# Performance work log

Measured on AMD Instinct MI355X. Metric: run time of the kernel, lower is better.

The kernel has to match this reference:

```python
import jax, jax.numpy as jnp
import numpy as np

LN_EPS = 1e-5
B, N, D, V = 2048, 8, 1024, 4096


def setup_inputs() -> dict:
    key = jax.random.key(0)
    k1, k2, k3, k4 = jax.random.split(key, 4)
    return {
        "input_embedding": jax.random.normal(k1, (B, D), dtype=jnp.float32),
        "features": jax.random.randint(k2, (B, N), 0, V, dtype=jnp.int64),
        "embed_tables": jax.random.normal(k3, (N, V, D), dtype=jnp.float32) * 0.02,
        "W_pred": jax.random.normal(k4, (N, D, V), dtype=jnp.float32) * 0.02,
        "b_pred": jnp.zeros((N, V), dtype=jnp.float32),
        "ln_gamma": jnp.ones((D,), dtype=jnp.float32),
        "ln_beta": jnp.zeros((D,), dtype=jnp.float32),
    }


def reference(input_embedding, features, embed_tables, W_pred, b_pred, ln_gamma, ln_beta):
    # Per-feature embedding lookup: embed_tables[n, features[b,n]] -> [B, N, D]
    feat_emb = embed_tables[jnp.arange(N)[None, :], features]
    # Stack input embedding in front: [B, N+1, D]
    embeddings = jnp.concatenate([input_embedding[:, None, :], feat_emb], axis=1)
    # Original: triu(diag=1) mask-multiply-sum then [:, 1:, :].
    # masked_sums[:, t] = sum_{s < t} emb[:, s]; slicing t=1..N == inclusive cumsum
    # over the first N positions.
    masked_sums = jnp.cumsum(embeddings, axis=1)[:, :-1, :]  # [B, N, D]
    # LayerNorm over last dim
    mu = jnp.mean(masked_sums, axis=-1, keepdims=True)
    var = jnp.var(masked_sums, axis=-1, keepdims=True)
    h = (masked_sums - mu) / jnp.sqrt(var + LN_EPS) * ln_gamma + ln_beta
    # Exact (erf) GELU, matching nn.GELU default
    h = jax.nn.gelu(h, approximate=False)
    # Per-feature predictor heads as one batched GEMM: [B, N, V]
    logits = jnp.einsum("bnd,ndv->bnv", h, W_pred) + b_pred
    return logits
```

## Files before the change

### kernel.cpp

```cpp
#include <hip/hip_runtime.h>
#include <hip/hip_bf16.h>

#define B_ 2048
#define N_ 8
#define D_ 1024
#define V_ 4096
#define LN_EPS_ 1e-5f

#define BM 128
#define BN 128
#define BK 32

typedef __bf16 bf16x8 __attribute__((ext_vector_type(8)));
typedef float f32x4 __attribute__((ext_vector_type(4)));

#define GLB(p) ((const __attribute__((address_space(1))) void*)(p))
#define LDSP(p) ((__attribute__((address_space(3))) void*)(p))

static __device__ __forceinline__ unsigned short f2bf(float x) {
    union { float f; unsigned int u; } v;
    v.f = x;
    unsigned int r = v.u + 0x7fffu + ((v.u >> 16) & 1u);
    return (unsigned short)(r >> 16);
}

__global__ __launch_bounds__(256) void wconv(const float* __restrict__ W,
                                             unsigned short* __restrict__ Wt) {
    __shared__ unsigned short tile[64][65];
    const int n  = blockIdx.z;
    const int v0 = blockIdx.x * 64;
    const int d0 = blockIdx.y * 64;
    const int tx = threadIdx.x;
    const int ty = threadIdx.y;
#pragma unroll
    for (int i = 0; i < 4; ++i) {
        const int d = ty + i * 16;
        const float4 w4 = *(const float4*)&W[((size_t)n * D_ + d0 + d) * V_ + v0 + tx * 4];
        tile[d][tx * 4 + 0] = f2bf(w4.x);
        tile[d][tx * 4 + 1] = f2bf(w4.y);
        tile[d][tx * 4 + 2] = f2bf(w4.z);
        tile[d][tx * 4 + 3] = f2bf(w4.w);
    }
    __syncthreads();
#pragma unroll
    for (int i = 0; i < 4; ++i) {
        const int v = ty + i * 16;
        ushort4 pk;
        pk.x = tile[tx * 4 + 0][v];
        pk.y = tile[tx * 4 + 1][v];
        pk.z = tile[tx * 4 + 2][v];
        pk.w = tile[tx * 4 + 3][v];
        *reinterpret_cast<ushort4*>(&Wt[((size_t)n * V_ + v0 + v) * D_ + d0 + tx * 4]) = pk;
    }
}

__global__ __launch_bounds__(256) void stage1(const float* __restrict__ ie,
                                              const int* __restrict__ feats,
                                              const float* __restrict__ emb,
                                              const float* __restrict__ gamma,
                                              const float* __restrict__ beta,
                                              unsigned short* __restrict__ H) {
    const int b = blockIdx.x;
    const int t = threadIdx.x;
    const int d0 = t * 4;
    const int lane = t & 63, wid = t >> 6;

    float4 s  = *(const float4*)&ie[(size_t)b * D_ + d0];
    const float4 g4 = *(const float4*)&gamma[d0];
    const float4 be4 = *(const float4*)&beta[d0];

    int fc[N_];
#pragma unroll
    for (int n = 0; n < N_; ++n) fc[n] = feats[b * N_ + n];

    __shared__ float redS[4], redQ[4];

#pragma unroll
    for (int n = 0; n < N_; ++n) {
        float ls = s.x + s.y + s.z + s.w;
        float lq = s.x * s.x + s.y * s.y + s.z * s.z + s.w * s.w;
#pragma unroll
        for (int off = 32; off > 0; off >>= 1) {
            ls += __shfl_down(ls, off, 64);
            lq += __shfl_down(lq, off, 64);
        }
        if (lane == 0) { redS[wid] = ls; redQ[wid] = lq; }
        __syncthreads();
        const float tot  = redS[0] + redS[1] + redS[2] + redS[3];
        const float totq = redQ[0] + redQ[1] + redQ[2] + redQ[3];
        __syncthreads();

        const float mu   = tot * (1.0f / D_);
        const float var  = totq * (1.0f / D_) - mu * mu;
        const float rstd = rsqrtf(var + LN_EPS_);

        float h0 = (s.x - mu) * rstd * g4.x + be4.x;
        float h1 = (s.y - mu) * rstd * g4.y + be4.y;
        float h2 = (s.z - mu) * rstd * g4.z + be4.z;
        float h3 = (s.w - mu) * rstd * g4.w + be4.w;
        h0 = 0.5f * h0 * (1.0f + erff(h0 * 0.70710678f));
        h1 = 0.5f * h1 * (1.0f + erff(h1 * 0.70710678f));
        h2 = 0.5f * h2 * (1.0f + erff(h2 * 0.70710678f));
        h3 = 0.5f * h3 * (1.0f + erff(h3 * 0.70710678f));

        ushort4 pk;
        pk.x = f2bf(h0); pk.y = f2bf(h1); pk.z = f2bf(h2); pk.w = f2bf(h3);
        *reinterpret_cast<ushort4*>(&H[((size_t)n * B_ + b) * D_ + d0]) = pk;

        const float4 e = *(const float4*)&emb[((size_t)n * V_ + fc[n]) * (size_t)D_ + d0];
        s.x += e.x; s.y += e.y; s.z += e.z; s.w += e.w;
    }
}

__global__ __launch_bounds__(256) void gemm(const unsigned short* __restrict__ H,
                                            const unsigned short* __restrict__ Wt,
                                            const float* __restrict__ bp,
                                            float* __restrict__ out) {
    const int vt = blockIdx.x;
    const int mt = blockIdx.y;
    const int n  = blockIdx.z;
    const int t = threadIdx.x;
    const int wid = t >> 6, lane = t & 63;
    const int wr = wid >> 1, wc = wid & 1;

    __shared__ unsigned short shA[BM * BK];
    __shared__ unsigned short shB[BN * BK];
    char* ldsA = (char*)shA;
    char* ldsB = (char*)shB;

    const unsigned short* Abase = H  + ((size_t)n * B_ + (size_t)mt * BM) * D_;
    const unsigned short* Bbase = Wt + ((size_t)n * V_ + (size_t)vt * BN) * D_;

    const int row0 = t >> 2;
    const int ks   = t & 3;

    f32x4 acc[4][4] = {};

    for (int kt = 0; kt < D_; kt += BK) {
        __builtin_amdgcn_global_load_lds(GLB(Abase + (size_t)row0 * D_ + kt + ks * 8),
                                         LDSP(ldsA + t * 16), 16, 0, 0);
        __builtin_amdgcn_global_load_lds(GLB(Abase + (size_t)(row0 + 64) * D_ + kt + ks * 8),
                                         LDSP(ldsA + 4096 + t * 16), 16, 0, 0);
        __builtin_amdgcn_global_load_lds(GLB(Bbase + (size_t)row0 * D_ + kt + ks * 8),
                                         LDSP(ldsB + t * 16), 16, 0, 0);
        __builtin_amdgcn_global_load_lds(GLB(Bbase + (size_t)(row0 + 64) * D_ + kt + ks * 8),
                                         LDSP(ldsB + 4096 + t * 16), 16, 0, 0);
        __syncthreads();

        const int lrow = lane & 15;
        const int lk   = (lane >> 4) * 16;
        bf16x8 af[4], bf[4];
#pragma unroll
        for (int i = 0; i < 4; ++i)
            af[i] = *reinterpret_cast<const bf16x8*>(ldsA + (wr * 64 + i * 16 + lrow) * 64 + lk);
#pragma unroll
        for (int i = 0; i < 4; ++i)
            bf[i] = *reinterpret_cast<const bf16x8*>(ldsB + (wc * 64 + i * 16 + lrow) * 64 + lk);
#pragma unroll
        for (int i = 0; i < 4; ++i)
#pragma unroll
            for (int j = 0; j < 4; ++j)
                acc[i][j] = __builtin_amdgcn_mfma_f32_16x16x32_bf16(af[i], bf[j], acc[i][j], 0, 0, 0);
        __syncthreads();
    }

    const int col  = lane & 15;
    const int rgrp = (lane >> 4) * 4;
    float bias[4];
#pragma unroll
    for (int j = 0; j < 4; ++j)
        bias[j] = bp[(size_t)n * V_ + vt * BN + wc * 64 + j * 16 + col];
#pragma unroll
    for (int i = 0; i < 4; ++i) {
        const int grow = mt * BM + wr * 64 + i * 16 + rgrp;
#pragma unroll
        for (int j = 0; j < 4; ++j) {
            const int gcol = vt * BN + wc * 64 + j * 16 + col;
#pragma unroll
            for (int r = 0; r < 4; ++r) {
                out[((size_t)(grow + r) * N_ + n) * V_ + gcol] = acc[i][j][r] + bias[j];
            }
        }
    }
}

extern "C" void kernel_launch(void* const* d_in, const int* in_sizes, int n_in,
                              void* d_out, int out_size, void* d_ws, size_t ws_size,
                              hipStream_t stream) {
    const float* ie  = (const float*)d_in[0];
    const int*   fts = (const int*)d_in[1];
    const float* emb = (const float*)d_in[2];
    const float* W   = (const float*)d_in[3];
    const float* bp  = (const float*)d_in[4];
    const float* gam = (const float*)d_in[5];
    const float* bet = (const float*)d_in[6];
    float* out = (float*)d_out;

    unsigned short* Wt = (unsigned short*)d_ws;
    unsigned short* H  = (unsigned short*)((char*)d_ws + (size_t)N_ * V_ * D_ * 2);

    wconv<<<dim3(V_ / 64, D_ / 64, N_), dim3(16, 16), 0, stream>>>(W, Wt);
    stage1<<<dim3(B_), dim3(256), 0, stream>>>(ie, fts, emb, gam, bet, H);
    gemm<<<dim3(V_ / BN, B_ / BM, N_), dim3(256), 0, stream>>>(H, Wt, bp, out);
}
```

Measured before the change: 284.5 us.

## Replace GEMM with 256x256 double-buffered, swizzled, 8-wave pipelined MFMA kernel

Swaps the simple 128x128x32 single-buffered GEMM for a 256x256x64 tile kernel with 512 threads. The kernel double-buffers through 128KB of dynamic LDS, issues the next tile's global-to-LDS loads interleaved with MFMA phases using explicit vmcnt waits and barriers, and XOR-swizzles the LDS layout to avoid bank conflicts. It also raises wave priority around MFMA blocks. The aim is to hide memory latency and raise arithmetic intensity, at the cost of more LDS, register pressure and fragile hand-placed wait counts.

```diff
diff --git a/kernel.cpp b/kernel.cpp
--- a/kernel.cpp
+++ b/kernel.cpp
@@ -6,10 +6,6 @@
 #define D_ 1024
 #define V_ 4096
 #define LN_EPS_ 1e-5f
-
-#define BM 128
-#define BN 128
-#define BK 32
 
 typedef __bf16 bf16x8 __attribute__((ext_vector_type(8)));
 typedef float f32x4 __attribute__((ext_vector_type(4)));
@@ -112,73 +108,123 @@
     }
 }
 
-__global__ __launch_bounds__(256) void gemm(const unsigned short* __restrict__ H,
-                                            const unsigned short* __restrict__ Wt,
-                                            const float* __restrict__ bp,
-                                            float* __restrict__ out) {
-    const int vt = blockIdx.x;
-    const int mt = blockIdx.y;
-    const int n  = blockIdx.z;
+#define MF(a, b, c) __builtin_amdgcn_mfma_f32_16x16x32_bf16((a), (b), (c), 0, 0, 0)
+
+#define STG_A(u, kt, bb) __builtin_amdgcn_global_load_lds( \
+    GLB(Ab + (size_t)((u) * 64 + srow) * D_ + (kt) + gsl), \
+    LDSP(lds + (bb) + (u) * 8192 + t * 16), 16, 0, 0)
+#define STG_B(u, kt, bb) __builtin_amdgcn_global_load_lds( \
+    GLB(Bb + (size_t)((u) * 64 + srow) * D_ + (kt) + gsl), \
+    LDSP(lds + (bb) + 32768 + (u) * 8192 + t * 16), 16, 0, 0)
+
+#define RD_A(i, ks, bb) (*(const bf16x8*)(lds + (bb) + ((i) >> 1) * 8192 + \
+    (((i) & 1) * 32 + wr * 16 + lrow) * 128 + ((((ks) * 4 + lkq) ^ sw) * 16)))
+#define RD_B(j, ks, bb) (*(const bf16x8*)(lds + (bb) + 32768 + wc * 8192 + \
+    ((j) * 16 + lrow) * 128 + ((((ks) * 4 + lkq) ^ sw) * 16)))
+
+#define QUADP(i0, i1) \
+    _Pragma("unroll") for (int j = 0; j < 4; ++j) { \
+        acc[i0][j] = MF(A00, Bf[j][0], acc[i0][j]); \
+        acc[i0][j] = MF(A01, Bf[j][1], acc[i0][j]); \
+        acc[i1][j] = MF(A10, Bf[j][0], acc[i1][j]); \
+        acc[i1][j] = MF(A11, Bf[j][1], acc[i1][j]); \
+    }
+
+#define TILE(KT, bc, bn) { \
+    bf16x8 Bf[4][2]; \
+    asm volatile("s_waitcnt vmcnt(3)" ::: "memory"); \
+    __builtin_amdgcn_s_barrier(); \
+    _Pragma("unroll") for (int j = 0; j < 4; ++j) { Bf[j][0] = RD_B(j, 0, bc); Bf[j][1] = RD_B(j, 1, bc); } \
+    { bf16x8 A00 = RD_A(0, 0, bc), A01 = RD_A(0, 1, bc), A10 = RD_A(1, 0, bc), A11 = RD_A(1, 1, bc); \
+      STG_B(0, (KT) + 64, bn); STG_B(1, (KT) + 64, bn); \
+      __builtin_amdgcn_s_setprio(1); QUADP(0, 1); __builtin_amdgcn_s_setprio(0); } \
+    asm volatile("s_waitcnt vmcnt(4)" ::: "memory"); \
+    __builtin_amdgcn_s_barrier(); \
+    { bf16x8 A00 = RD_A(2, 0, bc), A01 = RD_A(2, 1, bc), A10 = RD_A(3, 0, bc), A11 = RD_A(3, 1, bc); \
+      STG_B(2, (KT) + 64, bn); STG_B(3, (KT) + 64, bn); \
+      __builtin_amdgcn_s_setprio(1); QUADP(2, 3); __builtin_amdgcn_s_setprio(0); } \
+    asm volatile("s_waitcnt vmcnt(4)" ::: "memory"); \
+    __builtin_amdgcn_s_barrier(); \
+    { bf16x8 A00 = RD_A(4, 0, bc), A01 = RD_A(4, 1, bc), A10 = RD_A(5, 0, bc), A11 = RD_A(5, 1, bc); \
+      STG_A(0, (KT) + 64, bn); STG_A(1, (KT) + 64, bn); \
+      __builtin_amdgcn_s_setprio(1); QUADP(4, 5); __builtin_amdgcn_s_setprio(0); } \
+    asm volatile("s_waitcnt vmcnt(6)" ::: "memory"); \
+    __builtin_amdgcn_s_barrier(); \
+    { bf16x8 A00 = RD_A(6, 0, bc), A01 = RD_A(6, 1, bc), A10 = RD_A(7, 0, bc), A11 = RD_A(7, 1, bc); \
+      STG_A(2, (KT) + 64, bn); STG_A(3, (KT) + 64, bn); \
+      __builtin_amdgcn_s_setprio(1); QUADP(6, 7); __builtin_amdgcn_s_setprio(0); } \
+}
+
+#define TILE_LAST(bc) { \
+    bf16x8 Bf[4][2]; \
+    asm volatile("s_waitcnt vmcnt(3)" ::: "memory"); \
+    __builtin_amdgcn_s_barrier(); \
+    _Pragma("unroll") for (int j = 0; j < 4; ++j) { Bf[j][0] = RD_B(j, 0, bc); Bf[j][1] = RD_B(j, 1, bc); } \
+    { bf16x8 A00 = RD_A(0, 0, bc), A01 = RD_A(0, 1, bc), A10 = RD_A(1, 0, bc), A11 = RD_A(1, 1, bc); \
+      __builtin_amdgcn_s_setprio(1); QUADP(0, 1); __builtin_amdgcn_s_setprio(0); } \
+    asm volatile("s_waitcnt vmcnt(2)" ::: "memory"); \
+    __builtin_amdgcn_s_barrier(); \
+    { bf16x8 A00 = RD_A(2, 0, bc), A01 = RD_A(2, 1, bc), A10 = RD_A(3, 0, bc), A11 = RD_A(3, 1, bc); \
+      __builtin_amdgcn_s_setprio(1); QUADP(2, 3); __builtin_amdgcn_s_setprio(0); } \
+    asm volatile("s_waitcnt vmcnt(1)" ::: "memory"); \
+    __builtin_amdgcn_s_barrier(); \
+    { bf16x8 A00 = RD_A(4, 0, bc), A01 = RD_A(4, 1, bc), A10 = RD_A(5, 0, bc), A11 = RD_A(5, 1, bc); \
+      __builtin_amdgcn_s_setprio(1); QUADP(4, 5); __builtin_amdgcn_s_setprio(0); } \
+    asm volatile("s_waitcnt vmcnt(0)" ::: "memory"); \
+    __builtin_amdgcn_s_barrier(); \
+    { bf16x8 A00 = RD_A(6, 0, bc), A01 = RD_A(6, 1, bc), A10 = RD_A(7, 0, bc), A11 = RD_A(7, 1, bc); \
+      __builtin_amdgcn_s_setprio(1); QUADP(6, 7); __builtin_amdgcn_s_setprio(0); } \
+}
+
+__global__ __launch_bounds__(512, 2) void gemm8(const unsigned short* __restrict__ H,
+                                                const unsigned short* __restrict__ Wt,
+                                                const float* __restrict__ bp,
+                                                float* __restrict__ out) {
+    extern __shared__ char lds[];
+    const int vt = blockIdx.x, mt = blockIdx.y, n = blockIdx.z;
     const int t = threadIdx.x;
     const int wid = t >> 6, lane = t & 63;
-    const int wr = wid >> 1, wc = wid & 1;
-
-    __shared__ unsigned short shA[BM * BK];
-    __shared__ unsigned short shB[BN * BK];
-    char* ldsA = (char*)shA;
-    char* ldsB = (char*)shB;
-
-    const unsigned short* Abase = H  + ((size_t)n * B_ + (size_t)mt * BM) * D_;
-    const unsigned short* Bbase = Wt + ((size_t)n * V_ + (size_t)vt * BN) * D_;
-
-    const int row0 = t >> 2;
-    const int ks   = t & 3;
-
-    f32x4 acc[4][4] = {};
-
-    for (int kt = 0; kt < D_; kt += BK) {
-        __builtin_amdgcn_global_load_lds(GLB(Abase + (size_t)row0 * D_ + kt + ks * 8),
-                                         LDSP(ldsA + t * 16), 16, 0, 0);
-        __builtin_amdgcn_global_load_lds(GLB(Abase + (size_t)(row0 + 64) * D_ + kt + ks * 8),
-                                         LDSP(ldsA + 4096 + t * 16), 16, 0, 0);
-        __builtin_amdgcn_global_load_lds(GLB(Bbase + (size_t)row0 * D_ + kt + ks * 8),
-                                         LDSP(ldsB + t * 16), 16, 0, 0);
-        __builtin_amdgcn_global_load_lds(GLB(Bbase + (size_t)(row0 + 64) * D_ + kt + ks * 8),
-                                         LDSP(ldsB + 4096 + t * 16), 16, 0, 0);
-        __syncthreads();
-
-        const int lrow = lane & 15;
-        const int lk   = (lane >> 4) * 16;
-        bf16x8 af[4], bf[4];
-#pragma unroll
-        for (int i = 0; i < 4; ++i)
-            af[i] = *reinterpret_cast<const bf16x8*>(ldsA + (wr * 64 + i * 16 + lrow) * 64 + lk);
-#pragma unroll
-        for (int i = 0; i < 4; ++i)
-            bf[i] = *reinterpret_cast<const bf16x8*>(ldsB + (wc * 64 + i * 16 + lrow) * 64 + lk);
-#pragma unroll
-        for (int i = 0; i < 4; ++i)
-#pragma unroll
-            for (int j = 0; j < 4; ++j)
-                acc[i][j] = __builtin_amdgcn_mfma_f32_16x16x32_bf16(af[i], bf[j], acc[i][j], 0, 0, 0);
-        __syncthreads();
-    }
-
-    const int col  = lane & 15;
-    const int rgrp = (lane >> 4) * 4;
+    const int wr = wid >> 2, wc = wid & 3;
+
+    const unsigned short* Ab = H  + ((size_t)n * B_ + (size_t)mt * 256) * D_;
+    const unsigned short* Bb = Wt + ((size_t)n * V_ + (size_t)vt * 256) * D_;
+
+    const int srow = t >> 3;
+    const int gsl  = ((t & 7) ^ (srow & 7)) * 8;
+
+    const int lrow = lane & 15;
+    const int lkq  = lane >> 4;
+    const int sw   = lane & 7;
+
+    f32x4 acc[8][4] = {};
+
+    STG_B(0, 0, 0); STG_B(1, 0, 0); STG_B(2, 0, 0); STG_B(3, 0, 0);
+    STG_A(0, 0, 0); STG_A(1, 0, 0); STG_A(2, 0, 0); STG_A(3, 0, 0);
+
+    int kt = 0;
+#pragma unroll 1
+    for (int it = 0; it < 7; ++it) {
+        TILE(kt, 0, 65536); kt += 64;
+        TILE(kt, 65536, 0); kt += 64;
+    }
+    TILE(kt, 0, 65536);
+    TILE_LAST(65536);
+
+    const int col = lane & 15;
+    const int rg  = (lane >> 4) * 4;
+    const int gc0 = vt * 256 + wc * 64 + col;
     float bias[4];
 #pragma unroll
-    for (int j = 0; j < 4; ++j)
-        bias[j] = bp[(size_t)n * V_ + vt * BN + wc * 64 + j * 16 + col];
-#pragma unroll
-    for (int i = 0; i < 4; ++i) {
-        const int grow = mt * BM + wr * 64 + i * 16 + rgrp;
+    for (int j = 0; j < 4; ++j) bias[j] = bp[(size_t)n * V_ + gc0 + j * 16];
+#pragma unroll
+    for (int i = 0; i < 8; ++i) {
+        const int row = mt * 256 + i * 32 + wr * 16 + rg;
 #pragma unroll
         for (int j = 0; j < 4; ++j) {
-            const int gcol = vt * BN + wc * 64 + j * 16 + col;
+            const int gcol = gc0 + j * 16;
 #pragma unroll
             for (int r = 0; r < 4; ++r) {
-                out[((size_t)(grow + r) * N_ + n) * V_ + gcol] = acc[i][j][r] + bias[j];
+                out[((size_t)(row + r) * N_ + n) * V_ + gcol] = acc[i][j][r] + bias[j];
             }
         }
     }
@@ -199,7 +245,10 @@
     unsigned short* Wt = (unsigned short*)d_ws;
     unsigned short* H  = (unsigned short*)((char*)d_ws + (size_t)N_ * V_ * D_ * 2);
 
+    (void)hipFuncSetAttribute(reinterpret_cast<const void*>(gemm8),
+                              hipFuncAttributeMaxDynamicSharedMemorySize, 131072);
+
     wconv<<<dim3(V_ / 64, D_ / 64, N_), dim3(16, 16), 0, stream>>>(W, Wt);
     stage1<<<dim3(B_), dim3(256), 0, stream>>>(ie, fts, emb, gam, bet, H);
-    gemm<<<dim3(V_ / BN, B_ / BM, N_), dim3(256), 0, stream>>>(H, Wt, bp, out);
-}
+    gemm8<<<dim3(V_ / 256, B_ / 256, N_), 512, 131072, stream>>>(H, Wt, bp, out);
+}
```

New measurement: 254.0 us. -10.7%, faster.

## Fuse prep kernels and rewrite GEMM with 256x256 tiles and 4-stage LDS pipeline

Applied to the files above, without the earlier changes.

Merges the weight-conversion and LayerNorm/GELU kernels into one launch, using block-index ranges to pick the role. Replaces the 128x128 single-buffered GEMM with a 512-thread 256x256 tile kernel. The new GEMM keeps a 4-deep ring of direct-to-LDS loads with partial vmcnt waits, XOR-swizzles the LDS layout to avoid bank conflicts, raises MFMA issue priority, and remaps block IDs for better L2 locality. The aim is to hide global-memory latency and raise operand reuse, at the cost of 128KB of dynamic LDS per block and heavy register pressure.

```diff
diff --git a/kernel.cpp b/kernel.cpp
--- a/kernel.cpp
+++ b/kernel.cpp
@@ -7,10 +7,6 @@
 #define V_ 4096
 #define LN_EPS_ 1e-5f
 
-#define BM 128
-#define BN 128
-#define BK 32
-
 typedef __bf16 bf16x8 __attribute__((ext_vector_type(8)));
 typedef float f32x4 __attribute__((ext_vector_type(4)));
 
@@ -24,162 +20,189 @@
     return (unsigned short)(r >> 16);
 }
 
-__global__ __launch_bounds__(256) void wconv(const float* __restrict__ W,
-                                             unsigned short* __restrict__ Wt) {
-    __shared__ unsigned short tile[64][65];
-    const int n  = blockIdx.z;
-    const int v0 = blockIdx.x * 64;
-    const int d0 = blockIdx.y * 64;
-    const int tx = threadIdx.x;
-    const int ty = threadIdx.y;
-#pragma unroll
-    for (int i = 0; i < 4; ++i) {
-        const int d = ty + i * 16;
-        const float4 w4 = *(const float4*)&W[((size_t)n * D_ + d0 + d) * V_ + v0 + tx * 4];
-        tile[d][tx * 4 + 0] = f2bf(w4.x);
-        tile[d][tx * 4 + 1] = f2bf(w4.y);
-        tile[d][tx * 4 + 2] = f2bf(w4.z);
-        tile[d][tx * 4 + 3] = f2bf(w4.w);
+__global__ __launch_bounds__(256) void prep(const float* __restrict__ ie,
+                                            const int* __restrict__ feats,
+                                            const float* __restrict__ emb,
+                                            const float* __restrict__ gamma,
+                                            const float* __restrict__ beta,
+                                            const float* __restrict__ W,
+                                            unsigned short* __restrict__ H,
+                                            unsigned short* __restrict__ Wt) {
+    const int bid = blockIdx.x;
+    const int t = threadIdx.x;
+
+    if (bid >= 2048) {
+        __shared__ unsigned short tile[64][65];
+        const int w  = bid - 2048;
+        const int v0 = (w & 63) * 64;
+        const int d0 = ((w >> 6) & 15) * 64;
+        const int n  = w >> 10;
+        const int tx = t & 15, ty = t >> 4;
+#pragma unroll
+        for (int i = 0; i < 4; ++i) {
+            const int d = ty + i * 16;
+            const float4 w4 = *(const float4*)&W[((size_t)n * D_ + d0 + d) * V_ + v0 + tx * 4];
+            tile[d][tx * 4 + 0] = f2bf(w4.x);
+            tile[d][tx * 4 + 1] = f2bf(w4.y);
+            tile[d][tx * 4 + 2] = f2bf(w4.z);
+            tile[d][tx * 4 + 3] = f2bf(w4.w);
+        }
+        __syncthreads();
+#pragma unroll
+        for (int i = 0; i < 4; ++i) {
+            const int v = ty + i * 16;
+            ushort4 pk;
+            pk.x = tile[tx * 4 + 0][v];
+            pk.y = tile[tx * 4 + 1][v];
+            pk.z = tile[tx * 4 + 2][v];
+            pk.w = tile[tx * 4 + 3][v];
+            *reinterpret_cast<ushort4*>(&Wt[((size_t)n * V_ + v0 + v) * D_ + d0 + tx * 4]) = pk;
+        }
+    } else {
+        __shared__ float redS[4], redQ[4];
+        const int b = bid;
+        const int d0 = t * 4;
+        const int lane = t & 63, wid = t >> 6;
+
+        float4 s  = *(const float4*)&ie[(size_t)b * D_ + d0];
+        const float4 g4 = *(const float4*)&gamma[d0];
+        const float4 be4 = *(const float4*)&beta[d0];
+
+        int fc[N_];
+#pragma unroll
+        for (int n = 0; n < N_; ++n) fc[n] = feats[b * N_ + n];
+
+#pragma unroll
+        for (int n = 0; n < N_; ++n) {
+            float ls = s.x + s.y + s.z + s.w;
+            float lq = s.x * s.x + s.y * s.y + s.z * s.z + s.w * s.w;
+#pragma unroll
+            for (int off = 32; off > 0; off >>= 1) {
+                ls += __shfl_down(ls, off, 64);
+                lq += __shfl_down(lq, off, 64);
+            }
+            if (lane == 0) { redS[wid] = ls; redQ[wid] = lq; }
+            __syncthreads();
+            const float tot  = redS[0] + redS[1] + redS[2] + redS[3];
+            const float totq = redQ[0] + redQ[1] + redQ[2] + redQ[3];
+            __syncthreads();
+
+            const float mu   = tot * (1.0f / D_);
+            const float var  = totq * (1.0f / D_) - mu * mu;
+            const float rstd = rsqrtf(var + LN_EPS_);
+
+            float h0 = (s.x - mu) * rstd * g4.x + be4.x;
+            float h1 = (s.y - mu) * rstd * g4.y + be4.y;
+            float h2 = (s.z - mu) * rstd * g4.z + be4.z;
+            float h3 = (s.w - mu) * rstd * g4.w + be4.w;
+            h0 = 0.5f * h0 * (1.0f + erff(h0 * 0.70710678f));
+            h1 = 0.5f * h1 * (1.0f + erff(h1 * 0.70710678f));
+            h2 = 0.5f * h2 * (1.0f + erff(h2 * 0.70710678f));
+            h3 = 0.5f * h3 * (1.0f + erff(h3 * 0.70710678f));
+
+            ushort4 pk;
+            pk.x = f2bf(h0); pk.y = f2bf(h1); pk.z = f2bf(h2); pk.w = f2bf(h3);
+            *reinterpret_cast<ushort4*>(&H[((size_t)n * B_ + b) * D_ + d0]) = pk;
+
+            const float4 e = *(const float4*)&emb[((size_t)n * V_ + fc[n]) * (size_t)D_ + d0];
+            s.x += e.x; s.y += e.y; s.z += e.z; s.w += e.w;
+        }
     }
-    __syncthreads();
-#pragma unroll
-    for (int i = 0; i < 4; ++i) {
-        const int v = ty + i * 16;
-        ushort4 pk;
-        pk.x = tile[tx * 4 + 0][v];
-        pk.y = tile[tx * 4 + 1][v];
-        pk.z = tile[tx * 4 + 2][v];
-        pk.w = tile[tx * 4 + 3][v];
-        *reinterpret_cast<ushort4*>(&Wt[((size_t)n * V_ + v0 + v) * D_ + d0 + tx * 4]) = pk;
-    }
-}
-
-__global__ __launch_bounds__(256) void stage1(const float* __restrict__ ie,
-                                              const int* __restrict__ feats,
-                                              const float* __restrict__ emb,
-                                              const float* __restrict__ gamma,
-                                              const float* __restrict__ beta,
-                                              unsigned short* __restrict__ H) {
-    const int b = blockIdx.x;
-    const int t = threadIdx.x;
-    const int d0 = t * 4;
-    const int lane = t & 63, wid = t >> 6;
-
-    float4 s  = *(const float4*)&ie[(size_t)b * D_ + d0];
-    const float4 g4 = *(const float4*)&gamma[d0];
-    const float4 be4 = *(const float4*)&beta[d0];
-
-    int fc[N_];
-#pragma unroll
-    for (int n = 0; n < N_; ++n) fc[n] = feats[b * N_ + n];
-
-    __shared__ float redS[4], redQ[4];
-
-#pragma unroll
-    for (int n = 0; n < N_; ++n) {
-        float ls = s.x + s.y + s.z + s.w;
-        float lq = s.x * s.x + s.y * s.y + s.z * s.z + s.w * s.w;
-#pragma unroll
-        for (int off = 32; off > 0; off >>= 1) {
-            ls += __shfl_down(ls, off, 64);
-            lq += __shfl_down(lq, off, 64);
-        }
-        if (lane == 0) { redS[wid] = ls; redQ[wid] = lq; }
-        __syncthreads();
-        const float tot  = redS[0] + redS[1] + redS[2] + redS[3];
-        const float totq = redQ[0] + redQ[1] + redQ[2] + redQ[3];
-        __syncthreads();
-
-        const float mu   = tot * (1.0f / D_);
-        const float var  = totq * (1.0f / D_) - mu * mu;
-        const float rstd = rsqrtf(var + LN_EPS_);
-
-        float h0 = (s.x - mu) * rstd * g4.x + be4.x;
-        float h1 = (s.y - mu) * rstd * g4.y + be4.y;
-        float h2 = (s.z - mu) * rstd * g4.z + be4.z;
-        float h3 = (s.w - mu) * rstd * g4.w + be4.w;
-        h0 = 0.5f * h0 * (1.0f + erff(h0 * 0.70710678f));
-        h1 = 0.5f * h1 * (1.0f + erff(h1 * 0.70710678f));
-        h2 = 0.5f * h2 * (1.0f + erff(h2 * 0.70710678f));
-        h3 = 0.5f * h3 * (1.0f + erff(h3 * 0.70710678f));
-
-        ushort4 pk;
-        pk.x = f2bf(h0); pk.y = f2bf(h1); pk.z = f2bf(h2); pk.w = f2bf(h3);
-        *reinterpret_cast<ushort4*>(&H[((size_t)n * B_ + b) * D_ + d0]) = pk;
-
-        const float4 e = *(const float4*)&emb[((size_t)n * V_ + fc[n]) * (size_t)D_ + d0];
-        s.x += e.x; s.y += e.y; s.z += e.z; s.w += e.w;
-    }
-}
-
-__global__ __launch_bounds__(256) void gemm(const unsigned short* __restrict__ H,
-                                            const unsigned short* __restrict__ Wt,
-                                            const float* __restrict__ bp,
-                                            float* __restrict__ out) {
-    const int vt = blockIdx.x;
-    const int mt = blockIdx.y;
-    const int n  = blockIdx.z;
+}
+
+#define MF(a, b, c) __builtin_amdgcn_mfma_f32_16x16x32_bf16((a), (b), (c), 0, 0, 0)
+
+#define STAGE(As, Bs, bb) { \
+    __builtin_amdgcn_global_load_lds(GLB((As) + (size_t)srow * D_ + gsl),         LDSP(lds + (bb) + t * 16), 16, 0, 0); \
+    __builtin_amdgcn_global_load_lds(GLB((As) + (size_t)(srow + 128) * D_ + gsl), LDSP(lds + (bb) + 8192 + t * 16), 16, 0, 0); \
+    __builtin_amdgcn_global_load_lds(GLB((Bs) + (size_t)srow * D_ + gsl),         LDSP(lds + (bb) + 16384 + t * 16), 16, 0, 0); \
+    __builtin_amdgcn_global_load_lds(GLB((Bs) + (size_t)(srow + 128) * D_ + gsl), LDSP(lds + (bb) + 24576 + t * 16), 16, 0, 0); \
+}
+
+#define RD_A(i, bb) (*(const bf16x8*)(lds + (bb) + ((i) * 32 + wr * 16 + lrow) * 64 + swk))
+#define RD_B(j, bb) (*(const bf16x8*)(lds + (bb) + 16384 + (wc * 64 + (j) * 16 + lrow) * 64 + swk))
+
+#define TILE1(bc, bn, As, Bs) { \
+    asm volatile("s_waitcnt vmcnt(8)" ::: "memory"); \
+    __builtin_amdgcn_s_barrier(); \
+    STAGE(As, Bs, bn); \
+    bf16x8 Bf[4], Af[4]; \
+    _Pragma("unroll") for (int j = 0; j < 4; ++j) Bf[j] = RD_B(j, bc); \
+    _Pragma("unroll") for (int i = 0; i < 4; ++i) Af[i] = RD_A(i, bc); \
+    __builtin_amdgcn_s_setprio(1); \
+    _Pragma("unroll") for (int i = 0; i < 4; ++i) \
+        _Pragma("unroll") for (int j = 0; j < 4; ++j) \
+            acc[i][j] = MF(Af[i], Bf[j], acc[i][j]); \
+    __builtin_amdgcn_s_setprio(0); \
+    _Pragma("unroll") for (int i = 0; i < 4; ++i) Af[i] = RD_A((i) + 4, bc); \
+    __builtin_amdgcn_s_setprio(1); \
+    _Pragma("unroll") for (int i = 0; i < 4; ++i) \
+        _Pragma("unroll") for (int j = 0; j < 4; ++j) \
+            acc[i + 4][j] = MF(Af[i], Bf[j], acc[i + 4][j]); \
+    __builtin_amdgcn_s_setprio(0); \
+}
+
+__global__ __launch_bounds__(512, 2) void gemm4(const unsigned short* __restrict__ H,
+                                                const unsigned short* __restrict__ Wt,
+                                                const float* __restrict__ bp,
+                                                float* __restrict__ out) {
+    extern __shared__ char lds[];
+    const int bid = blockIdx.x;
+    const int logical = (bid & 7) * 128 + (bid >> 3);
+    const int n  = logical >> 7;
+    const int mt = (logical >> 4) & 7;
+    const int vt = logical & 15;
+
     const int t = threadIdx.x;
     const int wid = t >> 6, lane = t & 63;
-    const int wr = wid >> 1, wc = wid & 1;
-
-    __shared__ unsigned short shA[BM * BK];
-    __shared__ unsigned short shB[BN * BK];
-    char* ldsA = (char*)shA;
-    char* ldsB = (char*)shB;
-
-    const unsigned short* Abase = H  + ((size_t)n * B_ + (size_t)mt * BM) * D_;
-    const unsigned short* Bbase = Wt + ((size_t)n * V_ + (size_t)vt * BN) * D_;
-
-    const int row0 = t >> 2;
-    const int ks   = t & 3;
-
-    f32x4 acc[4][4] = {};
-
-    for (int kt = 0; kt < D_; kt += BK) {
-        __builtin_amdgcn_global_load_lds(GLB(Abase + (size_t)row0 * D_ + kt + ks * 8),
-                                         LDSP(ldsA + t * 16), 16, 0, 0);
-        __builtin_amdgcn_global_load_lds(GLB(Abase + (size_t)(row0 + 64) * D_ + kt + ks * 8),
-                                         LDSP(ldsA + 4096 + t * 16), 16, 0, 0);
-        __builtin_amdgcn_global_load_lds(GLB(Bbase + (size_t)row0 * D_ + kt + ks * 8),
-                                         LDSP(ldsB + t * 16), 16, 0, 0);
-        __builtin_amdgcn_global_load_lds(GLB(Bbase + (size_t)(row0 + 64) * D_ + kt + ks * 8),
-                                         LDSP(ldsB + 4096 + t * 16), 16, 0, 0);
-        __syncthreads();
-
-        const int lrow = lane & 15;
-        const int lk   = (lane >> 4) * 16;
-        bf16x8 af[4], bf[4];
-#pragma unroll
-        for (int i = 0; i < 4; ++i)
-            af[i] = *reinterpret_cast<const bf16x8*>(ldsA + (wr * 64 + i * 16 + lrow) * 64 + lk);
-#pragma unroll
-        for (int i = 0; i < 4; ++i)
-            bf[i] = *reinterpret_cast<const bf16x8*>(ldsB + (wc * 64 + i * 16 + lrow) * 64 + lk);
-#pragma unroll
-        for (int i = 0; i < 4; ++i)
-#pragma unroll
-            for (int j = 0; j < 4; ++j)
-                acc[i][j] = __builtin_amdgcn_mfma_f32_16x16x32_bf16(af[i], bf[j], acc[i][j], 0, 0, 0);
-        __syncthreads();
+    const int wr = wid >> 2, wc = wid & 3;
+
+    const unsigned short* Ab = H  + ((size_t)n * B_ + (size_t)mt * 256) * D_;
+    const unsigned short* Bb = Wt + ((size_t)n * V_ + (size_t)vt * 256) * D_;
+
+    const int srow = t >> 2;
+    const int gsl  = ((t & 3) ^ (srow & 3)) * 8;
+    const int lrow = lane & 15;
+    const int swk  = (((lane >> 4) ^ (lrow & 3))) * 16;
+    const int col  = lane & 15;
+    const int rg   = (lane >> 4) * 4;
+
+    float bias[4];
+#pragma unroll
+    for (int j = 0; j < 4; ++j)
+        bias[j] = bp[(size_t)n * V_ + vt * 256 + wc * 64 + j * 16 + col];
+    __builtin_amdgcn_sched_barrier(0);
+
+    f32x4 acc[8][4] = {};
+
+    STAGE(Ab, Bb, 0);
+    STAGE(Ab + 32, Bb + 32, 32768);
+    STAGE(Ab + 64, Bb + 64, 65536);
+
+#pragma unroll 1
+    for (int it = 0; it < 8; ++it) {
+        const int k0 = it * 128;
+        const int s0 = k0 + 96;
+        int s1 = k0 + 128; if (s1 >= 1024) s1 = 0;
+        int s2 = k0 + 160; if (s2 >= 1024) s2 = 0;
+        int s3 = k0 + 192; if (s3 >= 1024) s3 = 0;
+        TILE1(0,     98304, Ab + s0, Bb + s0);
+        TILE1(32768, 0,     Ab + s1, Bb + s1);
+        TILE1(65536, 32768, Ab + s2, Bb + s2);
+        TILE1(98304, 65536, Ab + s3, Bb + s3);
     }
-
-    const int col  = lane & 15;
-    const int rgrp = (lane >> 4) * 4;
-    float bias[4];
-#pragma unroll
-    for (int j = 0; j < 4; ++j)
-        bias[j] = bp[(size_t)n * V_ + vt * BN + wc * 64 + j * 16 + col];
-#pragma unroll
-    for (int i = 0; i < 4; ++i) {
-        const int grow = mt * BM + wr * 64 + i * 16 + rgrp;
+    asm volatile("s_waitcnt vmcnt(0)" ::: "memory");
+
+    const int gc0 = vt * 256 + wc * 64 + col;
+#pragma unroll
+    for (int i = 0; i < 8; ++i) {
+        const int row = mt * 256 + i * 32 + wr * 16 + rg;
 #pragma unroll
         for (int j = 0; j < 4; ++j) {
-            const int gcol = vt * BN + wc * 64 + j * 16 + col;
-#pragma unroll
-            for (int r = 0; r < 4; ++r) {
-                out[((size_t)(grow + r) * N_ + n) * V_ + gcol] = acc[i][j][r] + bias[j];
-            }
+            const int gcol = gc0 + j * 16;
+#pragma unroll
+            for (int r = 0; r < 4; ++r)
+                out[((size_t)(row + r) * N_ + n) * V_ + gcol] = acc[i][j][r] + bias[j];
         }
     }
 }
@@ -199,7 +222,9 @@
     unsigned short* Wt = (unsigned short*)d_ws;
     unsigned short* H  = (unsigned short*)((char*)d_ws + (size_t)N_ * V_ * D_ * 2);
 
-    wconv<<<dim3(V_ / 64, D_ / 64, N_), dim3(16, 16), 0, stream>>>(W, Wt);
-    stage1<<<dim3(B_), dim3(256), 0, stream>>>(ie, fts, emb, gam, bet, H);
-    gemm<<<dim3(V_ / BN, B_ / BM, N_), dim3(256), 0, stream>>>(H, Wt, bp, out);
-}
+    (void)hipFuncSetAttribute(reinterpret_cast<const void*>(gemm4),
+                              hipFuncAttributeMaxDynamicSharedMemorySize, 131072);
+
+    prep<<<dim3(2048 + 8192), dim3(256), 0, stream>>>(ie, fts, emb, gam, bet, W, H, Wt);
+    gemm4<<<dim3(1024), dim3(512), 131072, stream>>>(H, Wt, bp, out);
+}
```

Result: faster. 244.4 us (-14.1%).
